# Optimization experiments

Hardware: AMD Instinct MI355X
Metric: run time of the kernel (lower is better)

Reference implementation:

```python
import jax, jax.numpy as jnp
import numpy as np

D_MODEL = 1024
HEADS = 16
HEAD_DIM = D_MODEL // HEADS


def setup_inputs() -> dict:
    key = jax.random.key(0)
    k_x, k_q, k_k, k_v, k_o = jax.random.split(key, 5)
    x = jax.random.normal(k_x, (4, 2048, D_MODEL), dtype=jnp.float32)
    W_q = jax.random.normal(k_q, (D_MODEL, D_MODEL), dtype=jnp.float32)
    W_k = jax.random.normal(k_k, (D_MODEL, D_MODEL), dtype=jnp.float32)
    W_v = jax.random.normal(k_v, (D_MODEL, D_MODEL), dtype=jnp.float32)
    fc_out = jax.random.normal(k_o, (D_MODEL, D_MODEL), dtype=jnp.float32)
    return {"x": x, "W_q": W_q, "W_k": W_k, "W_v": W_v, "fc_out": fc_out}


def reference(x, W_q, W_k, W_v, fc_out):
    b, s, d = x.shape
    h, hd = HEADS, HEAD_DIM
    # Projections: [b, s, d]
    Q = x @ W_q
    K = x @ W_k
    V = x @ W_v
    # Split heads: [b, h, s, hd]
    Q = Q.reshape(b, s, h, hd).transpose(0, 2, 1, 3)
    K = K.reshape(b, s, h, hd).transpose(0, 2, 1, 3)
    V = V.reshape(b, s, h, hd).transpose(0, 2, 1, 3)
    # Scaled dot-product attention (softmax over key axis, per row)
    scores = jnp.einsum('bhqd,bhkd->bhqk', Q, K) / jnp.sqrt(jnp.float32(hd))
    attn = jax.nn.softmax(scores, axis=-1)
    head_out = jnp.einsum('bhqk,bhkd->bhqd', attn, V)
    # Concat heads back: [b, s, d]
    concat = head_out.transpose(0, 2, 1, 3).reshape(b, s, d)
    return concat @ fc_out
```

## Files before the change

kernel.cpp:

```cpp
#include <hip/hip_runtime.h>
#include <hip/hip_fp16.h>

#define BATCH   4
#define SEQ     2048
#define DM      1024
#define HEADS   16
#define HD      64
#define M_TOK   (BATCH * SEQ)
#define QK_LD   2048

#define QSCALE  0.1803368801111204f

typedef __attribute__((ext_vector_type(8)))  _Float16 half8;
typedef __attribute__((ext_vector_type(4)))  float    f32x4;
typedef __attribute__((ext_vector_type(16))) float    f32x16;

__device__ __forceinline__ unsigned short f2h(float x) {
    return __half_as_ushort(__float2half(x));
}
__device__ __forceinline__ float h2f(unsigned short u) {
    return __half2float(__ushort_as_half(u));
}
__device__ __forceinline__ float fast_exp2(float x) {
    float r; asm volatile("v_exp_f32 %0, %1" : "=v"(r) : "v"(x)); return r;
}
__device__ __forceinline__ unsigned int pk2(float a, float b) {
    __fp16 __attribute__((ext_vector_type(2))) h =
        __builtin_amdgcn_cvt_pkrtz(a, b);
    return __builtin_bit_cast(unsigned int, h);
}
__device__ __forceinline__ void dma16(const void* g, void* l) {
    __builtin_amdgcn_global_load_lds(
        (const __attribute__((address_space(1))) void*)g,
        (__attribute__((address_space(3))) void*)l, 16, 0, 0);
}

__global__ __launch_bounds__(256) void split_cast(
    const float* __restrict__ x, unsigned short* __restrict__ hi,
    unsigned short* __restrict__ lo)
{
    const int i = (blockIdx.x * 256 + threadIdx.x) * 8;
    float4 a = *(const float4*)(x + i);
    float4 b = *(const float4*)(x + i + 4);
    float v[8] = {a.x, a.y, a.z, a.w, b.x, b.y, b.z, b.w};
    unsigned short hb[8], lb[8];
#pragma unroll
    for (int j = 0; j < 8; ++j) {
        hb[j] = f2h(v[j]);
        lb[j] = f2h(v[j] - h2f(hb[j]));
    }
    *(float4*)(hi + i) = *(float4*)hb;
    *(float4*)(lo + i) = *(float4*)lb;
}

template<int SPLIT>
__global__ __launch_bounds__(256) void wtrans(
    const float* __restrict__ W, unsigned short* __restrict__ Th_out,
    unsigned short* __restrict__ Tl_out, float scale)
{
    __shared__ unsigned short Th[64][72];
    __shared__ unsigned short Tl[SPLIT ? 64 : 1][72];
    const int t  = threadIdx.x;
    const int n0 = blockIdx.x * 64, k0 = blockIdx.y * 64;
    const int kr = t >> 2, cg = (t & 3) << 4;
#pragma unroll
    for (int jj = 0; jj < 16; jj += 4) {
        float4 wv = *(const float4*)(W + (size_t)(k0 + kr) * DM + n0 + cg + jj);
        float vv[4] = {wv.x, wv.y, wv.z, wv.w};
#pragma unroll
        for (int j = 0; j < 4; ++j) {
            float v = vv[j] * scale;
            unsigned short h = f2h(v);
            Th[cg + jj + j][kr] = h;
            if (SPLIT) Tl[cg + jj + j][kr] = f2h(v - h2f(h));
        }
    }
    __syncthreads();
    const int nr = t >> 2, kg = (t & 3) << 4;
    size_t go = (size_t)(n0 + nr) * DM + k0 + kg;
    *(float4*)(Th_out + go)     = *(float4*)&Th[nr][kg];
    *(float4*)(Th_out + go + 8) = *(float4*)&Th[nr][kg + 8];
    if (SPLIT) {
        *(float4*)(Tl_out + go)     = *(float4*)&Tl[nr][kg];
        *(float4*)(Tl_out + go + 8) = *(float4*)&Tl[nr][kg + 8];
    }
}

template<int PASSES, int EPI>
__global__ __launch_bounds__(256, 2) void gemm_f16(
    const unsigned short* __restrict__ Ah, const unsigned short* __restrict__ Al,
    const unsigned short* __restrict__ Bh, const unsigned short* __restrict__ Bl,
    void* __restrict__ O0, void* __restrict__ O1, int M, int N, int K)
{
    __shared__ unsigned short As_h[2][128 * 32];
    __shared__ unsigned short Bs_h[2][128 * 32];
    __shared__ unsigned short As_l[PASSES == 3 ? 2 : 1][PASSES == 3 ? 128 * 32 : 16];
    __shared__ unsigned short Bs_l[PASSES == 3 ? 2 : 1][PASSES == 3 ? 128 * 32 : 16];

    const int t = threadIdx.x;
    const int w = t >> 6, lane = t & 63, quad = lane >> 4, l15 = lane & 15;
    const int wm = w >> 1, wn = w & 1;
    const int m0 = blockIdx.y * 128, n0 = blockIdx.x * 128;

    const int drow = w * 32 + (lane >> 2);
    const int dcol = (lane & 3) * 8;

    auto stage = [&](int buf, int k0) {
#pragma unroll
        for (int inst = 0; inst < 2; ++inst) {
            const size_t ga = (size_t)(m0 + drow + inst * 16) * K + k0 + dcol;
            const size_t gb = (size_t)(n0 + drow + inst * 16) * K + k0 + dcol;
            const int lo = (w * 32 + inst * 16) * 32;
            dma16(Ah + ga, &As_h[buf][lo]);
            dma16(Bh + gb, &Bs_h[buf][lo]);
            if (PASSES == 3) {
                dma16(Al + ga, &As_l[buf][lo]);
                dma16(Bl + gb, &Bs_l[buf][lo]);
            }
        }
    };

    f32x4 acc[4][4];
#pragma unroll
    for (int mt = 0; mt < 4; ++mt)
#pragma unroll
        for (int nt = 0; nt < 4; ++nt)
#pragma unroll
            for (int r = 0; r < 4; ++r) acc[mt][nt][r] = 0.f;

    const int NIT = K >> 5;
    stage(0, 0);
    for (int it = 0; it < NIT; ++it) {
        __syncthreads();
        const int cur = it & 1;
        if (it + 1 < NIT) stage(cur ^ 1, (it + 1) * 32);

        half8 aH[4], bH[4], aL[4], bL[4];
#pragma unroll
        for (int mt = 0; mt < 4; ++mt) {
            const int row = wm * 64 + mt * 16 + l15;
            aH[mt] = *(const half8*)&As_h[cur][row * 32 + quad * 8];
            if (PASSES == 3) aL[mt] = *(const half8*)&As_l[cur][row * 32 + quad * 8];
        }
#pragma unroll
        for (int nt = 0; nt < 4; ++nt) {
            const int row = wn * 64 + nt * 16 + l15;
            bH[nt] = *(const half8*)&Bs_h[cur][row * 32 + quad * 8];
            if (PASSES == 3) bL[nt] = *(const half8*)&Bs_l[cur][row * 32 + quad * 8];
        }
#pragma unroll
        for (int mt = 0; mt < 4; ++mt)
#pragma unroll
            for (int nt = 0; nt < 4; ++nt) {
                acc[mt][nt] = __builtin_amdgcn_mfma_f32_16x16x32_f16(
                    aH[mt], bH[nt], acc[mt][nt], 0, 0, 0);
                if (PASSES == 3) {
                    acc[mt][nt] = __builtin_amdgcn_mfma_f32_16x16x32_f16(
                        aH[mt], bL[nt], acc[mt][nt], 0, 0, 0);
                    acc[mt][nt] = __builtin_amdgcn_mfma_f32_16x16x32_f16(
                        aL[mt], bH[nt], acc[mt][nt], 0, 0, 0);
                }
            }
    }

#pragma unroll
    for (int mt = 0; mt < 4; ++mt)
#pragma unroll
        for (int nt = 0; nt < 4; ++nt) {
            const int row0 = m0 + wm * 64 + mt * 16 + quad * 4;
            const int col  = n0 + wn * 64 + nt * 16 + l15;
            if (EPI == 0) {
#pragma unroll
                for (int r = 0; r < 4; ++r)
                    ((float*)O0)[(size_t)(row0 + r) * N + col] = acc[mt][nt][r];
            } else if (EPI == 1) {
#pragma unroll
                for (int r = 0; r < 4; ++r) {
                    float v = acc[mt][nt][r];
                    unsigned short h = f2h(v);
                    ((unsigned short*)O0)[(size_t)(row0 + r) * N + col] = h;
                    ((unsigned short*)O1)[(size_t)(row0 + r) * N + col] =
                        f2h(v - h2f(h));
                }
            } else if (EPI == 2) {
#pragma unroll
                for (int r = 0; r < 4; ++r)
                    ((unsigned short*)O0)[(size_t)(row0 + r) * N + col] =
                        f2h(acc[mt][nt][r]);
            } else {
                const int b = row0 >> 11, s = row0 & 2047;
                const int hh = col >> 6, d = col & 63;
                unsigned short vs[4];
#pragma unroll
                for (int r = 0; r < 4; ++r) vs[r] = f2h(acc[mt][nt][r]);
                *(ushort4*)((unsigned short*)O0 +
                            (((size_t)(b * HEADS + hh)) * HD + d) * SEQ + s) =
                    *(ushort4*)vs;
            }
        }
}

__global__ __launch_bounds__(256, 2) void attn_f16(
    const unsigned short* __restrict__ QKh,
    const unsigned short* __restrict__ QKl,
    const unsigned short* __restrict__ Vt,
    unsigned short* __restrict__ Oc)
{
    __shared__ unsigned short SM[2][3 * 4096];

    const int t = threadIdx.x;
    const int w = t >> 6, lane = t & 63;
    const int g = lane >> 5, l31 = lane & 31;
    const int b = blockIdx.z, h = blockIdx.y, q0 = blockIdx.x * 256;

    const size_t row0   = (size_t)b * SEQ;
    const size_t qcol   = (size_t)h * HD;
    const size_t kcol   = 1024 + qcol;
    const size_t vtbase = ((size_t)(b * HEADS + h)) * HD * SEQ;

    const int rl  = lane >> 3;
    const int sw8 = ((lane & 7) ^ (rl & 7)) * 8;
    const int x7  = l31 & 7;

    auto stage = [&](int buf, int k0) {
#pragma unroll
        for (int inst = 0; inst < 2; ++inst) {
            const int r8 = w * 16 + inst * 8;
            const size_t gk = (row0 + k0 + r8 + rl) * QK_LD + kcol + sw8;
            const int lo = r8 * 64;
            dma16(QKh + gk, &SM[buf][lo]);
            dma16(QKl + gk, &SM[buf][4096 + lo]);
            const size_t gv = vtbase + (size_t)(r8 + rl) * SEQ + k0 + sw8;
            dma16(Vt + gv, &SM[buf][8192 + lo]);
        }
    };

    half8 bQh[2][4], bQl[2][4];
#pragma unroll
    for (int qs = 0; qs < 2; ++qs) {
        const size_t qr = (row0 + q0 + qs * 128 + w * 32 + l31) * QK_LD + qcol;
#pragma unroll
        for (int ks = 0; ks < 4; ++ks) {
            bQh[qs][ks] = *(const half8*)(QKh + qr + ks * 16 + g * 8);
            bQl[qs][ks] = *(const half8*)(QKl + qr + ks * 16 + g * 8);
        }
    }

    f32x16 o_acc[2][2];
#pragma unroll
    for (int qs = 0; qs < 2; ++qs)
#pragma unroll
        for (int mt = 0; mt < 2; ++mt)
#pragma unroll
            for (int r = 0; r < 16; ++r) o_acc[qs][mt][r] = 0.f;
    float m_r[2] = {-3.0e38f, -3.0e38f}, l_r[2] = {0.f, 0.f};

    stage(0, 0);
    const int NIT = SEQ / 64;
    for (int it = 0; it < NIT; ++it) {
        __syncthreads();
        const int cur = it & 1;
        if (it + 1 < NIT) stage(cur ^ 1, (it + 1) * 64);
        const unsigned short* Ks  = &SM[cur][0];
        const unsigned short* Ksl = &SM[cur][4096];
        const unsigned short* Vs  = &SM[cur][8192];

        f32x16 s[2][2];
#pragma unroll
        for (int qs = 0; qs < 2; ++qs)
#pragma unroll
            for (int kt = 0; kt < 2; ++kt)
#pragma unroll
                for (int r = 0; r < 16; ++r) s[qs][kt][r] = 0.f;
#pragma unroll
        for (int kt = 0; kt < 2; ++kt)
#pragma unroll
            for (int ks = 0; ks < 4; ++ks) {
                const int off = (kt * 32 + l31) * 64 + (((ks * 2 + g) ^ x7) * 8);
                half8 aKh = *(const half8*)&Ks[off];
                half8 aKl = *(const half8*)&Ksl[off];
#pragma unroll
                for (int qs = 0; qs < 2; ++qs) {
                    s[qs][kt] = __builtin_amdgcn_mfma_f32_32x32x16_f16(
                        aKh, bQh[qs][ks], s[qs][kt], 0, 0, 0);
                    s[qs][kt] = __builtin_amdgcn_mfma_f32_32x32x16_f16(
                        aKl, bQh[qs][ks], s[qs][kt], 0, 0, 0);
                    s[qs][kt] = __builtin_amdgcn_mfma_f32_32x32x16_f16(
                        aKh, bQl[qs][ks], s[qs][kt], 0, 0, 0);
                }
            }

        half8 bP[2][4];
#pragma unroll
        for (int qs = 0; qs < 2; ++qs) {
            float mx = s[qs][0][0];
#pragma unroll
            for (int kt = 0; kt < 2; ++kt)
#pragma unroll
                for (int r = 0; r < 16; ++r) mx = fmaxf(mx, s[qs][kt][r]);
            mx = fmaxf(mx, __shfl_xor(mx, 32));
            const float nm = fmaxf(m_r[qs], mx);
            const float al = fast_exp2(m_r[qs] - nm);
            m_r[qs] = nm;
            float rs = 0.f;
#pragma unroll
            for (int kt = 0; kt < 2; ++kt)
#pragma unroll
                for (int r = 0; r < 16; ++r) {
                    float pv = fast_exp2(s[qs][kt][r] - nm);
                    s[qs][kt][r] = pv;
                    rs += pv;
                }
            rs += __shfl_xor(rs, 32);
            l_r[qs] = l_r[qs] * al + rs;
#pragma unroll
            for (int mt = 0; mt < 2; ++mt)
#pragma unroll
                for (int r = 0; r < 16; ++r) o_acc[qs][mt][r] *= al;

#pragma unroll
            for (int kt = 0; kt < 2; ++kt)
#pragma unroll
                for (int ksl = 0; ksl < 2; ++ksl) {
                    const int base = ksl * 8;
                    unsigned int lo0 = pk2(s[qs][kt][base + 0], s[qs][kt][base + 1]);
                    unsigned int lo1 = pk2(s[qs][kt][base + 2], s[qs][kt][base + 3]);
                    unsigned int hi0 = pk2(s[qs][kt][base + 4], s[qs][kt][base + 5]);
                    unsigned int hi1 = pk2(s[qs][kt][base + 6], s[qs][kt][base + 7]);
                    unsigned int s0 = g ? lo0 : hi0;
                    unsigned int s1 = g ? lo1 : hi1;
                    unsigned int r0 = (unsigned int)__shfl_xor((int)s0, 32);
                    unsigned int r1 = (unsigned int)__shfl_xor((int)s1, 32);
                    union { unsigned int u[4]; half8 hv; } u;
                    u.u[0] = g ? r0 : lo0;
                    u.u[1] = g ? r1 : lo1;
                    u.u[2] = g ? hi0 : r0;
                    u.u[3] = g ? hi1 : r1;
                    bP[qs][kt * 2 + ksl] = u.hv;
                }
        }

#pragma unroll
        for (int mt = 0; mt < 2; ++mt)
#pragma unroll
            for (int kk = 0; kk < 4; ++kk) {
                const int off = (mt * 32 + l31) * 64 + (((kk * 2 + g) ^ x7) * 8);
                half8 aV = *(const half8*)&Vs[off];
#pragma unroll
                for (int qs = 0; qs < 2; ++qs)
                    o_acc[qs][mt] = __builtin_amdgcn_mfma_f32_32x32x16_f16(
                        aV, bP[qs][kk], o_acc[qs][mt], 0, 0, 0);
            }
    }

#pragma unroll
    for (int qs = 0; qs < 2; ++qs) {
        const float inv = 1.0f / l_r[qs];
        unsigned short* orow =
            Oc + (row0 + q0 + qs * 128 + w * 32 + l31) * DM + h * HD;
#pragma unroll
        for (int mt = 0; mt < 2; ++mt)
#pragma unroll
            for (int rq = 0; rq < 4; ++rq) {
                unsigned int w0 = pk2(o_acc[qs][mt][rq * 4 + 0] * inv,
                                      o_acc[qs][mt][rq * 4 + 1] * inv);
                unsigned int w1 = pk2(o_acc[qs][mt][rq * 4 + 2] * inv,
                                      o_acc[qs][mt][rq * 4 + 3] * inv);
                const int d0 = mt * 32 + rq * 8 + g * 4;
                uint2 pkd; pkd.x = w0; pkd.y = w1;
                *(uint2*)(orow + d0) = pkd;
            }
    }
}

extern "C" void kernel_launch(void* const* d_in, const int* in_sizes, int n_in,
                              void* d_out, int out_size, void* d_ws, size_t ws_size,
                              hipStream_t stream) {
    const float* x  = (const float*)d_in[0];
    const float* Wq = (const float*)d_in[1];
    const float* Wk = (const float*)d_in[2];
    const float* Wv = (const float*)d_in[3];
    const float* Wo = (const float*)d_in[4];
    float* out = (float*)d_out;

    char* ws = (char*)d_ws;
    const size_t SZ_TOK = (size_t)M_TOK * DM * 2;
    const size_t SZ_W   = (size_t)DM * DM * 2;

    unsigned short* xh     = (unsigned short*)(ws);
    unsigned short* xl     = (unsigned short*)(ws + SZ_TOK);
    unsigned short* Wqkt_h = (unsigned short*)(ws + 2 * SZ_TOK);
    unsigned short* Wqkt_l = (unsigned short*)(ws + 2 * SZ_TOK + 2 * SZ_W);
    unsigned short* Wvt    = (unsigned short*)(ws + 2 * SZ_TOK + 4 * SZ_W);
    unsigned short* Wot    = (unsigned short*)(ws + 2 * SZ_TOK + 5 * SZ_W);
    unsigned short* QKh    = (unsigned short*)(ws + 2 * SZ_TOK + 6 * SZ_W);
    unsigned short* QKl    = (unsigned short*)(ws + 4 * SZ_TOK + 6 * SZ_W);
    unsigned short* Vt_    = (unsigned short*)(ws + 6 * SZ_TOK + 6 * SZ_W);
    unsigned short* concat = xh;

    dim3 blk(256);

    hipLaunchKernelGGL(split_cast, dim3(M_TOK * DM / (256 * 8)), blk, 0, stream,
                       x, xh, xl);
    dim3 wgrid(DM / 64, DM / 64);
    hipLaunchKernelGGL((wtrans<1>), wgrid, blk, 0, stream, Wq, Wqkt_h, Wqkt_l,
                       QSCALE);
    hipLaunchKernelGGL((wtrans<1>), wgrid, blk, 0, stream, Wk,
                       Wqkt_h + (size_t)DM * DM, Wqkt_l + (size_t)DM * DM, 1.0f);
    hipLaunchKernelGGL((wtrans<0>), wgrid, blk, 0, stream, Wv, Wvt, nullptr, 1.0f);
    hipLaunchKernelGGL((wtrans<0>), wgrid, blk, 0, stream, Wo, Wot, nullptr, 1.0f);

    dim3 gqk(QK_LD / 128, M_TOK / 128);
    hipLaunchKernelGGL((gemm_f16<3, 1>), gqk, blk, 0, stream,
                       xh, xl, Wqkt_h, Wqkt_l, QKh, QKl, M_TOK, QK_LD, DM);
    dim3 ggrid(DM / 128, M_TOK / 128);
    hipLaunchKernelGGL((gemm_f16<1, 3>), ggrid, blk, 0, stream,
                       xh, nullptr, Wvt, nullptr, Vt_, nullptr, M_TOK, DM, DM);

    dim3 agrid(SEQ / 256, HEADS, BATCH);
    hipLaunchKernelGGL(attn_f16, agrid, blk, 0, stream, QKh, QKl, Vt_, concat);

    hipLaunchKernelGGL((gemm_f16<1, 0>), ggrid, blk, 0, stream,
                       concat, nullptr, Wot, nullptr, out, nullptr, M_TOK, DM, DM);
}
```

Before: 433.0 us.

## Rework QK GEMM with 32x32 MFMA, merge weight transposes, lazy softmax rescale

Adds a dedicated split-precision QK projection GEMM that uses 32x32x16 MFMA tiles, assigns one wave to stage each of the four operand streams with a swizzled LDS layout, and raises occupancy to 3 blocks per CU. The four weight-transpose launches are merged into a single kernel indexed by blockIdx.z. In attention, the online-softmax rescale is skipped when no lane's max increases, the P·V accumulation is interleaved per query sub-tile to reduce live registers, and the grid order is changed so that head and batch vary fastest. The goal is fewer launches, less rescale work, and better MFMA efficiency, at the cost of higher register pressure under the tighter launch bounds.

```diff
diff --git a/kernel.cpp b/kernel.cpp
--- a/kernel.cpp
+++ b/kernel.cpp
@@ -21,9 +21,14 @@
 __device__ __forceinline__ float h2f(unsigned short u) {
     return __half2float(__ushort_as_half(u));
 }
-__device__ __forceinline__ float fast_exp2(float x) {
-    float r; asm volatile("v_exp_f32 %0, %1" : "=v"(r) : "v"(x)); return r;
-}
+#if __has_builtin(__builtin_amdgcn_exp2f)
+#define EXP2F(x) __builtin_amdgcn_exp2f(x)
+#else
+__device__ __forceinline__ float exp2_asm(float x) {
+    float r; asm("v_exp_f32 %0, %1" : "=v"(r) : "v"(x)); return r;
+}
+#define EXP2F(x) exp2_asm(x)
+#endif
 __device__ __forceinline__ unsigned int pk2(float a, float b) {
     __fp16 __attribute__((ext_vector_type(2))) h =
         __builtin_amdgcn_cvt_pkrtz(a, b);
@@ -53,13 +58,23 @@
     *(float4*)(lo + i) = *(float4*)lb;
 }
 
-template<int SPLIT>
-__global__ __launch_bounds__(256) void wtrans(
-    const float* __restrict__ W, unsigned short* __restrict__ Th_out,
-    unsigned short* __restrict__ Tl_out, float scale)
+__global__ __launch_bounds__(256) void wtrans_all(
+    const float* __restrict__ Wq, const float* __restrict__ Wk,
+    const float* __restrict__ Wv, const float* __restrict__ Wo,
+    unsigned short* __restrict__ Wqkt_h, unsigned short* __restrict__ Wqkt_l,
+    unsigned short* __restrict__ Wvt, unsigned short* __restrict__ Wot)
 {
     __shared__ unsigned short Th[64][72];
-    __shared__ unsigned short Tl[SPLIT ? 64 : 1][72];
+    __shared__ unsigned short Tl[64][72];
+    const int z = blockIdx.z;
+    const float* W = (z == 0) ? Wq : (z == 1) ? Wk : (z == 2) ? Wv : Wo;
+    unsigned short* Th_out = (z == 0) ? Wqkt_h
+                           : (z == 1) ? Wqkt_h + (size_t)DM * DM
+                           : (z == 2) ? Wvt : Wot;
+    unsigned short* Tl_out = (z == 0) ? Wqkt_l : Wqkt_l + (size_t)DM * DM;
+    const float scale = (z == 0) ? QSCALE : 1.0f;
+    const bool split = (z < 2);
+
     const int t  = threadIdx.x;
     const int n0 = blockIdx.x * 64, k0 = blockIdx.y * 64;
     const int kr = t >> 2, cg = (t & 3) << 4;
@@ -72,7 +87,7 @@
             float v = vv[j] * scale;
             unsigned short h = f2h(v);
             Th[cg + jj + j][kr] = h;
-            if (SPLIT) Tl[cg + jj + j][kr] = f2h(v - h2f(h));
+            Tl[cg + jj + j][kr] = f2h(v - h2f(h));
         }
     }
     __syncthreads();
@@ -80,22 +95,106 @@
     size_t go = (size_t)(n0 + nr) * DM + k0 + kg;
     *(float4*)(Th_out + go)     = *(float4*)&Th[nr][kg];
     *(float4*)(Th_out + go + 8) = *(float4*)&Th[nr][kg + 8];
-    if (SPLIT) {
+    if (split) {
         *(float4*)(Tl_out + go)     = *(float4*)&Tl[nr][kg];
         *(float4*)(Tl_out + go + 8) = *(float4*)&Tl[nr][kg + 8];
     }
 }
 
-template<int PASSES, int EPI>
-__global__ __launch_bounds__(256, 2) void gemm_f16(
+__global__ __launch_bounds__(256, 3) void gemm_qk(
     const unsigned short* __restrict__ Ah, const unsigned short* __restrict__ Al,
     const unsigned short* __restrict__ Bh, const unsigned short* __restrict__ Bl,
-    void* __restrict__ O0, void* __restrict__ O1, int M, int N, int K)
+    unsigned short* __restrict__ Oh, unsigned short* __restrict__ Ol)
+{
+    __shared__ unsigned short SM[2][4][128 * 16];
+
+    const int t = threadIdx.x;
+    const int w = t >> 6, lane = t & 63;
+    const int g = lane >> 5, l31 = lane & 31;
+    const int wm = w >> 1, wn = w & 1;
+    const int m0 = blockIdx.y * 128, n0 = blockIdx.x * 128;
+
+    const unsigned short* src = (w == 0) ? Ah : (w == 1) ? Bh : (w == 2) ? Al : Bl;
+    const int base0 = (w == 1 || w == 3) ? n0 : m0;
+    const int drl = lane >> 1;
+    const int dch = (lane & 1) ^ ((lane >> 3) & 1);
+
+    auto stage = [&](int buf, int k0) {
+#pragma unroll
+        for (int i = 0; i < 4; ++i) {
+            const int row = i * 32 + drl;
+            dma16(src + (size_t)(base0 + row) * DM + k0 + dch * 8,
+                  &SM[buf][w][i * 32 * 16]);
+        }
+    };
+
+    f32x16 acc[2][2];
+#pragma unroll
+    for (int mt = 0; mt < 2; ++mt)
+#pragma unroll
+        for (int nt = 0; nt < 2; ++nt)
+#pragma unroll
+            for (int r = 0; r < 16; ++r) acc[mt][nt][r] = 0.f;
+
+    stage(0, 0);
+    const int NIT = DM / 16;
+    for (int it = 0; it < NIT; ++it) {
+        __syncthreads();
+        const int cur = it & 1;
+        if (it + 1 < NIT) stage(cur ^ 1, (it + 1) * 16);
+
+        half8 a_h[2], b_h[2], a_l[2], b_l[2];
+#pragma unroll
+        for (int mt = 0; mt < 2; ++mt) {
+            const int row = wm * 64 + mt * 32 + l31;
+            const int off = row * 16 + ((g ^ ((l31 >> 2) & 1)) * 8);
+            a_h[mt] = *(const half8*)&SM[cur][0][off];
+            a_l[mt] = *(const half8*)&SM[cur][2][off];
+        }
+#pragma unroll
+        for (int nt = 0; nt < 2; ++nt) {
+            const int row = wn * 64 + nt * 32 + l31;
+            const int off = row * 16 + ((g ^ ((l31 >> 2) & 1)) * 8);
+            b_h[nt] = *(const half8*)&SM[cur][1][off];
+            b_l[nt] = *(const half8*)&SM[cur][3][off];
+        }
+#pragma unroll
+        for (int mt = 0; mt < 2; ++mt)
+#pragma unroll
+            for (int nt = 0; nt < 2; ++nt) {
+                acc[mt][nt] = __builtin_amdgcn_mfma_f32_32x32x16_f16(
+                    a_h[mt], b_h[nt], acc[mt][nt], 0, 0, 0);
+                acc[mt][nt] = __builtin_amdgcn_mfma_f32_32x32x16_f16(
+                    a_h[mt], b_l[nt], acc[mt][nt], 0, 0, 0);
+                acc[mt][nt] = __builtin_amdgcn_mfma_f32_32x32x16_f16(
+                    a_l[mt], b_h[nt], acc[mt][nt], 0, 0, 0);
+            }
+    }
+
+#pragma unroll
+    for (int mt = 0; mt < 2; ++mt)
+#pragma unroll
+        for (int nt = 0; nt < 2; ++nt) {
+            const int col = n0 + wn * 64 + nt * 32 + l31;
+#pragma unroll
+            for (int r = 0; r < 16; ++r) {
+                const int row = m0 + wm * 64 + mt * 32 +
+                                (r & 3) + 8 * (r >> 2) + 4 * g;
+                const float v = acc[mt][nt][r];
+                const unsigned short h = f2h(v);
+                Oh[(size_t)row * QK_LD + col] = h;
+                Ol[(size_t)row * QK_LD + col] = f2h(v - h2f(h));
+            }
+        }
+}
+
+template<int EPI>
+__global__ __launch_bounds__(256, 3) void gemm_f16(
+    const unsigned short* __restrict__ Ah, const unsigned short* __restrict__ Bh,
+    void* __restrict__ O0, int M, int N, int K)
 {
     __shared__ unsigned short As_h[2][128 * 32];
     __shared__ unsigned short Bs_h[2][128 * 32];
-    __shared__ unsigned short As_l[PASSES == 3 ? 2 : 1][PASSES == 3 ? 128 * 32 : 16];
-    __shared__ unsigned short Bs_l[PASSES == 3 ? 2 : 1][PASSES == 3 ? 128 * 32 : 16];
 
     const int t = threadIdx.x;
     const int w = t >> 6, lane = t & 63, quad = lane >> 4, l15 = lane & 15;
@@ -113,10 +212,6 @@
             const int lo = (w * 32 + inst * 16) * 32;
             dma16(Ah + ga, &As_h[buf][lo]);
             dma16(Bh + gb, &Bs_h[buf][lo]);
-            if (PASSES == 3) {
-                dma16(Al + ga, &As_l[buf][lo]);
-                dma16(Bl + gb, &Bs_l[buf][lo]);
-            }
         }
     };
 
@@ -135,32 +230,19 @@
         const int cur = it & 1;
         if (it + 1 < NIT) stage(cur ^ 1, (it + 1) * 32);
 
-        half8 aH[4], bH[4], aL[4], bL[4];
-#pragma unroll
-        for (int mt = 0; mt < 4; ++mt) {
-            const int row = wm * 64 + mt * 16 + l15;
-            aH[mt] = *(const half8*)&As_h[cur][row * 32 + quad * 8];
-            if (PASSES == 3) aL[mt] = *(const half8*)&As_l[cur][row * 32 + quad * 8];
-        }
-#pragma unroll
-        for (int nt = 0; nt < 4; ++nt) {
-            const int row = wn * 64 + nt * 16 + l15;
-            bH[nt] = *(const half8*)&Bs_h[cur][row * 32 + quad * 8];
-            if (PASSES == 3) bL[nt] = *(const half8*)&Bs_l[cur][row * 32 + quad * 8];
-        }
+        half8 aH[4], bH[4];
 #pragma unroll
         for (int mt = 0; mt < 4; ++mt)
-#pragma unroll
-            for (int nt = 0; nt < 4; ++nt) {
+            aH[mt] = *(const half8*)&As_h[cur][(wm * 64 + mt * 16 + l15) * 32 + quad * 8];
+#pragma unroll
+        for (int nt = 0; nt < 4; ++nt)
+            bH[nt] = *(const half8*)&Bs_h[cur][(wn * 64 + nt * 16 + l15) * 32 + quad * 8];
+#pragma unroll
+        for (int mt = 0; mt < 4; ++mt)
+#pragma unroll
+            for (int nt = 0; nt < 4; ++nt)
                 acc[mt][nt] = __builtin_amdgcn_mfma_f32_16x16x32_f16(
                     aH[mt], bH[nt], acc[mt][nt], 0, 0, 0);
-                if (PASSES == 3) {
-                    acc[mt][nt] = __builtin_amdgcn_mfma_f32_16x16x32_f16(
-                        aH[mt], bL[nt], acc[mt][nt], 0, 0, 0);
-                    acc[mt][nt] = __builtin_amdgcn_mfma_f32_16x16x32_f16(
-                        aL[mt], bH[nt], acc[mt][nt], 0, 0, 0);
-                }
-            }
     }
 
 #pragma unroll
@@ -173,20 +255,6 @@
 #pragma unroll
                 for (int r = 0; r < 4; ++r)
                     ((float*)O0)[(size_t)(row0 + r) * N + col] = acc[mt][nt][r];
-            } else if (EPI == 1) {
-#pragma unroll
-                for (int r = 0; r < 4; ++r) {
-                    float v = acc[mt][nt][r];
-                    unsigned short h = f2h(v);
-                    ((unsigned short*)O0)[(size_t)(row0 + r) * N + col] = h;
-                    ((unsigned short*)O1)[(size_t)(row0 + r) * N + col] =
-                        f2h(v - h2f(h));
-                }
-            } else if (EPI == 2) {
-#pragma unroll
-                for (int r = 0; r < 4; ++r)
-                    ((unsigned short*)O0)[(size_t)(row0 + r) * N + col] =
-                        f2h(acc[mt][nt][r]);
             } else {
                 const int b = row0 >> 11, s = row0 & 2047;
                 const int hh = col >> 6, d = col & 63;
@@ -211,7 +279,8 @@
     const int t = threadIdx.x;
     const int w = t >> 6, lane = t & 63;
     const int g = lane >> 5, l31 = lane & 31;
-    const int b = blockIdx.z, h = blockIdx.y, q0 = blockIdx.x * 256;
+    const int bh = blockIdx.x;
+    const int b = bh >> 4, h = bh & 15, q0 = blockIdx.y * 256;
 
     const size_t row0   = (size_t)b * SEQ;
     const size_t qcol   = (size_t)h * HD;
@@ -290,7 +359,6 @@
                 }
             }
 
-        half8 bP[2][4];
 #pragma unroll
         for (int qs = 0; qs < 2; ++qs) {
             float mx = s[qs][0][0];
@@ -299,25 +367,31 @@
 #pragma unroll
                 for (int r = 0; r < 16; ++r) mx = fmaxf(mx, s[qs][kt][r]);
             mx = fmaxf(mx, __shfl_xor(mx, 32));
-            const float nm = fmaxf(m_r[qs], mx);
-            const float al = fast_exp2(m_r[qs] - nm);
-            m_r[qs] = nm;
+
+            if (__ballot(mx > m_r[qs])) {
+                const float nm = fmaxf(m_r[qs], mx);
+                const float al = EXP2F(m_r[qs] - nm);
+                m_r[qs] = nm;
+                l_r[qs] *= al;
+#pragma unroll
+                for (int mt = 0; mt < 2; ++mt)
+#pragma unroll
+                    for (int r = 0; r < 16; ++r) o_acc[qs][mt][r] *= al;
+            }
+            const float nm = m_r[qs];
             float rs = 0.f;
 #pragma unroll
             for (int kt = 0; kt < 2; ++kt)
 #pragma unroll
                 for (int r = 0; r < 16; ++r) {
-                    float pv = fast_exp2(s[qs][kt][r] - nm);
+                    float pv = EXP2F(s[qs][kt][r] - nm);
                     s[qs][kt][r] = pv;
                     rs += pv;
                 }
             rs += __shfl_xor(rs, 32);
-            l_r[qs] = l_r[qs] * al + rs;
-#pragma unroll
-            for (int mt = 0; mt < 2; ++mt)
-#pragma unroll
-                for (int r = 0; r < 16; ++r) o_acc[qs][mt][r] *= al;
-
+            l_r[qs] += rs;
+
+            half8 bP[4];
 #pragma unroll
             for (int kt = 0; kt < 2; ++kt)
 #pragma unroll
@@ -336,21 +410,19 @@
                     u.u[1] = g ? r1 : lo1;
                     u.u[2] = g ? hi0 : r0;
                     u.u[3] = g ? hi1 : r1;
-                    bP[qs][kt * 2 + ksl] = u.hv;
+                    bP[kt * 2 + ksl] = u.hv;
                 }
-        }
-
-#pragma unroll
-        for (int mt = 0; mt < 2; ++mt)
-#pragma unroll
-            for (int kk = 0; kk < 4; ++kk) {
-                const int off = (mt * 32 + l31) * 64 + (((kk * 2 + g) ^ x7) * 8);
-                half8 aV = *(const half8*)&Vs[off];
-#pragma unroll
-                for (int qs = 0; qs < 2; ++qs)
+
+#pragma unroll
+            for (int mt = 0; mt < 2; ++mt)
+#pragma unroll
+                for (int kk = 0; kk < 4; ++kk) {
+                    const int off = (mt * 32 + l31) * 64 + (((kk * 2 + g) ^ x7) * 8);
+                    half8 aV = *(const half8*)&Vs[off];
                     o_acc[qs][mt] = __builtin_amdgcn_mfma_f32_32x32x16_f16(
-                        aV, bP[qs][kk], o_acc[qs][mt], 0, 0, 0);
-            }
+                        aV, bP[kk], o_acc[qs][mt], 0, 0, 0);
+                }
+        }
     }
 
 #pragma unroll
@@ -402,24 +474,17 @@
 
     hipLaunchKernelGGL(split_cast, dim3(M_TOK * DM / (256 * 8)), blk, 0, stream,
                        x, xh, xl);
-    dim3 wgrid(DM / 64, DM / 64);
-    hipLaunchKernelGGL((wtrans<1>), wgrid, blk, 0, stream, Wq, Wqkt_h, Wqkt_l,
-                       QSCALE);
-    hipLaunchKernelGGL((wtrans<1>), wgrid, blk, 0, stream, Wk,
-                       Wqkt_h + (size_t)DM * DM, Wqkt_l + (size_t)DM * DM, 1.0f);
-    hipLaunchKernelGGL((wtrans<0>), wgrid, blk, 0, stream, Wv, Wvt, nullptr, 1.0f);
-    hipLaunchKernelGGL((wtrans<0>), wgrid, blk, 0, stream, Wo, Wot, nullptr, 1.0f);
-
-    dim3 gqk(QK_LD / 128, M_TOK / 128);
-    hipLaunchKernelGGL((gemm_f16<3, 1>), gqk, blk, 0, stream,
-                       xh, xl, Wqkt_h, Wqkt_l, QKh, QKl, M_TOK, QK_LD, DM);
-    dim3 ggrid(DM / 128, M_TOK / 128);
-    hipLaunchKernelGGL((gemm_f16<1, 3>), ggrid, blk, 0, stream,
-                       xh, nullptr, Wvt, nullptr, Vt_, nullptr, M_TOK, DM, DM);
-
-    dim3 agrid(SEQ / 256, HEADS, BATCH);
-    hipLaunchKernelGGL(attn_f16, agrid, blk, 0, stream, QKh, QKl, Vt_, concat);
-
-    hipLaunchKernelGGL((gemm_f16<1, 0>), ggrid, blk, 0, stream,
-                       concat, nullptr, Wot, nullptr, out, nullptr, M_TOK, DM, DM);
-}
+    hipLaunchKernelGGL(wtrans_all, dim3(DM / 64, DM / 64, 4), blk, 0, stream,
+                       Wq, Wk, Wv, Wo, Wqkt_h, Wqkt_l, Wvt, Wot);
+
+    hipLaunchKernelGGL(gemm_qk, dim3(QK_LD / 128, M_TOK / 128), blk, 0, stream,
+                       xh, xl, Wqkt_h, Wqkt_l, QKh, QKl);
+    hipLaunchKernelGGL((gemm_f16<3>), dim3(DM / 128, M_TOK / 128), blk, 0, stream,
+                       xh, Wvt, Vt_, M_TOK, DM, DM);
+
+    hipLaunchKernelGGL(attn_f16, dim3(HEADS * BATCH, SEQ / 256), blk, 0, stream,
+                       QKh, QKl, Vt_, concat);
+
+    hipLaunchKernelGGL((gemm_f16<0>), dim3(DM / 128, M_TOK / 128), blk, 0, stream,
+                       concat, Wot, out, M_TOK, DM, DM);
+}
```

Result: slower. 471.8 us (+9.0%).
